# Kernel optimization log

Hardware: AMD Instinct MI355X
Metric: run time of the kernel (lower is better)

## Reference

```python
import jax, jax.numpy as jnp
import numpy as np

N = 50000
NEG_SLOPE = 0.2


def _gat_layer(x, src, dst, W, a_src, a_dst, b, heads, out_ch, concat):
    # x: [N, F_in]; W: [F_in, heads*out_ch]; a_src/a_dst: [heads, out_ch]; b: bias
    h = (x @ W).reshape(N, heads, out_ch)                      # [N,H,C]
    s_src = jnp.einsum('nhc,hc->nh', h, a_src)                 # [N,H]
    s_dst = jnp.einsum('nhc,hc->nh', h, a_dst)                 # [N,H]
    e = jax.nn.leaky_relu(s_src[src] + s_dst[dst], NEG_SLOPE)  # [E,H]
    # segment softmax over edges sharing the same destination node
    m = jax.ops.segment_max(e, dst, num_segments=N)
    m = jax.lax.stop_gradient(jnp.where(jnp.isfinite(m), m, 0.0))
    w = jnp.exp(e - m[dst])
    denom = jax.ops.segment_sum(w, dst, num_segments=N)
    alpha = w / (denom[dst] + 1e-16)                           # [E,H]
    out = jax.ops.segment_sum(alpha[:, :, None] * h[src], dst, num_segments=N)  # [N,H,C]
    out = out.reshape(N, heads * out_ch) if concat else out.mean(axis=1)
    return out + b


def setup_inputs() -> dict:
    key = jax.random.key(0)
    ks = jax.random.split(key, 16)
    F_in, Hd, H1, H3, F_out = 128, 64, 4, 6, 64
    E = 800000
    x = jax.random.normal(ks[0], (N, F_in), dtype=jnp.float32)
    edge_index = jax.random.randint(ks[1], (2, E), 0, N, dtype=jnp.int64)

    def glorot(k, shape, fan_in):
        return jax.random.normal(k, shape, dtype=jnp.float32) * (1.0 / np.sqrt(fan_in))

    params = {
        'W1': glorot(ks[2], (F_in, H1 * Hd), F_in),
        'a1_src': glorot(ks[3], (H1, Hd), Hd),
        'a1_dst': glorot(ks[4], (H1, Hd), Hd),
        'b1': jnp.zeros((H1 * Hd,), dtype=jnp.float32),
        'W2': glorot(ks[5], (H1 * Hd, H1 * Hd), H1 * Hd),
        'a2_src': glorot(ks[6], (H1, Hd), Hd),
        'a2_dst': glorot(ks[7], (H1, Hd), Hd),
        'b2': jnp.zeros((H1 * Hd,), dtype=jnp.float32),
        'W3': glorot(ks[8], (H1 * Hd, H3 * F_out), H1 * Hd),
        'a3_src': glorot(ks[9], (H3, F_out), F_out),
        'a3_dst': glorot(ks[10], (H3, F_out), F_out),
        'b3': jnp.zeros((F_out,), dtype=jnp.float32),
    }
    return {'x': x, 'edge_index': edge_index, **params}


def reference(x, edge_index, W1, a1_src, a1_dst, b1, W2, a2_src, a2_dst, b2, W3, a3_src, a3_dst, b3):
    # PyG GATConv default add_self_loops=True
    loops = jnp.arange(N, dtype=edge_index.dtype)
    src = jnp.concatenate([edge_index[0], loops])
    dst = jnp.concatenate([edge_index[1], loops])
    x1 = jax.nn.elu(_gat_layer(x, src, dst, W1, a1_src, a1_dst, b1, heads=4, out_ch=64, concat=True))
    x2 = jax.nn.elu(_gat_layer(x1, src, dst, W2, a2_src, a2_dst, b2, heads=4, out_ch=64, concat=True))
    x3 = _gat_layer(x2, src, dst, W3, a3_src, a3_dst, b3, heads=6, out_ch=64, concat=False)
    return x3
```

## Files before the change

kernel.cpp:

```cpp
#include <hip/hip_runtime.h>
#include <hip/hip_bf16.h>
#include <hip/hip_fp16.h>
#include <math.h>

#define NNODES 50000

typedef __attribute__((ext_vector_type(8))) short short8v;
typedef __attribute__((ext_vector_type(4))) float f32x4;
typedef unsigned short ushort_t;
typedef unsigned int uint_t;

__device__ inline ushort_t f2bf_bits(float v) {
    union { __hip_bfloat16 b; ushort_t u; } c;
    c.b = __float2bfloat16(v);
    return c.u;
}
__device__ inline float bfbits2f(ushort_t u) {
    union { __hip_bfloat16 b; ushort_t u; } c;
    c.u = u;
    return __bfloat162float(c.b);
}
__device__ inline ushort_t f2h_bits(float v) {
    union { __half h; ushort_t u; } c;
    c.h = __float2half(v);
    return c.u;
}
__device__ inline void cvt2(uint_t u, float& a, float& b) {
    union { uint_t u; __half2 h; } c; c.u = u;
    a = __low2float(c.h); b = __high2float(c.h);
}
__device__ inline uint_t fmap(float f) {
    uint_t b = __float_as_uint(f);
    return (b & 0x80000000u) ? ~b : (b | 0x80000000u);
}
__device__ inline float funmap(uint_t u) {
    return __uint_as_float((u & 0x80000000u) ? (u & 0x7FFFFFFFu) : ~u);
}

__global__ __launch_bounds__(256)
void split_kernel(const float4* __restrict__ in, ushort4* __restrict__ hi,
                  ushort4* __restrict__ lo, int n4) {
    int i = blockIdx.x * blockDim.x + threadIdx.x;
    if (i >= n4) return;
    float4 v = in[i];
    ushort4 h, l;
    h.x = f2bf_bits(v.x); l.x = f2bf_bits(v.x - bfbits2f(h.x));
    h.y = f2bf_bits(v.y); l.y = f2bf_bits(v.y - bfbits2f(h.y));
    h.z = f2bf_bits(v.z); l.z = f2bf_bits(v.z - bfbits2f(h.z));
    h.w = f2bf_bits(v.w); l.w = f2bf_bits(v.w - bfbits2f(h.w));
    hi[i] = h; lo[i] = l;
}

__global__ __launch_bounds__(256)
void wprep_all(const float* __restrict__ W1, const float* __restrict__ W2,
               const float* __restrict__ W3,
               ushort_t* __restrict__ w1h, ushort_t* __restrict__ w1l,
               ushort_t* __restrict__ w2h, ushort_t* __restrict__ w2l,
               ushort_t* __restrict__ w3h, ushort_t* __restrict__ w3l) {
    int idx = blockIdx.x * blockDim.x + threadIdx.x;
    const float* W; ushort_t* hT; ushort_t* lT; int K, N;
    if (idx < 128 * 256) { W = W1; hT = w1h; lT = w1l; K = 128; N = 256; }
    else if (idx < 128 * 256 + 256 * 256) {
        idx -= 128 * 256; W = W2; hT = w2h; lT = w2l; K = 256; N = 256;
    } else {
        idx -= 128 * 256 + 256 * 256;
        if (idx >= 256 * 384) return;
        W = W3; hT = w3h; lT = w3l; K = 256; N = 384;
    }
    int k = idx / N, n = idx - k * N;
    float v = W[idx];
    ushort_t hb = f2bf_bits(v);
    hT[(size_t)n * K + k] = hb;
    lT[(size_t)n * K + k] = f2bf_bits(v - bfbits2f(hb));
}

template<int H>
__global__ __launch_bounds__(256)
void gemm_fused(const ushort_t* __restrict__ Ahi, const ushort_t* __restrict__ Alo,
                const ushort_t* __restrict__ Bhi, const ushort_t* __restrict__ Blo,
                ushort_t* __restrict__ h16, float* __restrict__ ssrc,
                float* __restrict__ sdst, uint_t* __restrict__ gmaxu,
                const float* __restrict__ a_src, const float* __restrict__ a_dst,
                int M, int K) {
    __shared__ char smem[32768];
    __shared__ float sSs[128][2], sDs[128][2];
    __shared__ uint_t gblk[2];

    const int tid = threadIdx.x;
    const int lane = tid & 63;
    const int wid = tid >> 6;
    const int wm = wid >> 1, wn = wid & 1;
    const int bm = blockIdx.y * 128;
    const int bn = blockIdx.x * 128;
    const int r15 = lane & 15;
    const int g4 = lane >> 4;

    if (tid < 128) { sSs[tid][0] = 0.f; sSs[tid][1] = 0.f;
                     sDs[tid][0] = 0.f; sDs[tid][1] = 0.f; }
    if (tid < 2) gblk[tid] = 0;

    char* As_hi = smem;
    char* As_lo = smem + 8192;
    char* Bs_hi = smem + 16384;
    char* Bs_lo = smem + 24576;

    const int srow = tid >> 1;
    const int sch  = (tid & 1) * 2;
    const size_t arow = (size_t)(bm + srow) * K;
    const size_t brow = (size_t)(bn + srow) * K;

    f32x4 acc[4][4] = {};

    for (int k0 = 0; k0 < K; k0 += 32) {
        short8v a0 = *(const short8v*)&Ahi[arow + k0 + sch * 8];
        short8v a1 = *(const short8v*)&Ahi[arow + k0 + sch * 8 + 8];
        short8v l0 = *(const short8v*)&Alo[arow + k0 + sch * 8];
        short8v l1 = *(const short8v*)&Alo[arow + k0 + sch * 8 + 8];
        short8v b0 = *(const short8v*)&Bhi[brow + k0 + sch * 8];
        short8v b1 = *(const short8v*)&Bhi[brow + k0 + sch * 8 + 8];
        short8v m0 = *(const short8v*)&Blo[brow + k0 + sch * 8];
        short8v m1 = *(const short8v*)&Blo[brow + k0 + sch * 8 + 8];
        __syncthreads();
        *(short8v*)(As_hi + sch * 2048 + srow * 16)       = a0;
        *(short8v*)(As_hi + (sch + 1) * 2048 + srow * 16) = a1;
        *(short8v*)(As_lo + sch * 2048 + srow * 16)       = l0;
        *(short8v*)(As_lo + (sch + 1) * 2048 + srow * 16) = l1;
        *(short8v*)(Bs_hi + sch * 2048 + srow * 16)       = b0;
        *(short8v*)(Bs_hi + (sch + 1) * 2048 + srow * 16) = b1;
        *(short8v*)(Bs_lo + sch * 2048 + srow * 16)       = m0;
        *(short8v*)(Bs_lo + (sch + 1) * 2048 + srow * 16) = m1;
        __syncthreads();

        short8v ah[4], al[4], bh[4], bl[4];
        #pragma unroll
        for (int mi = 0; mi < 4; ++mi) {
            int row = wm * 64 + mi * 16 + r15;
            ah[mi] = *(const short8v*)(As_hi + g4 * 2048 + row * 16);
            al[mi] = *(const short8v*)(As_lo + g4 * 2048 + row * 16);
        }
        #pragma unroll
        for (int nj = 0; nj < 4; ++nj) {
            int row = wn * 64 + nj * 16 + r15;
            bh[nj] = *(const short8v*)(Bs_hi + g4 * 2048 + row * 16);
            bl[nj] = *(const short8v*)(Bs_lo + g4 * 2048 + row * 16);
        }
        #pragma unroll
        for (int mi = 0; mi < 4; ++mi)
            #pragma unroll
            for (int nj = 0; nj < 4; ++nj) {
                acc[mi][nj] = __builtin_amdgcn_mfma_f32_16x16x32_bf16(ah[mi], bh[nj], acc[mi][nj], 0, 0, 0);
                acc[mi][nj] = __builtin_amdgcn_mfma_f32_16x16x32_bf16(ah[mi], bl[nj], acc[mi][nj], 0, 0, 0);
                acc[mi][nj] = __builtin_amdgcn_mfma_f32_16x16x32_bf16(al[mi], bh[nj], acc[mi][nj], 0, 0, 0);
            }
    }
    __syncthreads();

    ushort_t* h2 = (ushort_t*)smem;
    const int headg = (bn >> 6) + wn;
    float asv[4], adv[4];
    #pragma unroll
    for (int nj = 0; nj < 4; ++nj) {
        asv[nj] = a_src[headg * 64 + nj * 16 + r15];
        adv[nj] = a_dst[headg * 64 + nj * 16 + r15];
    }
    #pragma unroll
    for (int mi = 0; mi < 4; ++mi) {
        #pragma unroll
        for (int reg = 0; reg < 4; ++reg) {
            int row_l = wm * 64 + mi * 16 + g4 * 4 + reg;
            int csw = ((row_l >> 2) & 3) << 2;
            float pS = 0.f, pD = 0.f;
            #pragma unroll
            for (int nj = 0; nj < 4; ++nj) {
                float v = acc[mi][nj][reg];
                int col_l = wn * 64 + nj * 16 + r15;
                h2[row_l * 128 + (col_l ^ csw)] = f2h_bits(v);
                pS += v * asv[nj];
                pD += v * adv[nj];
            }
            #pragma unroll
            for (int off = 1; off < 16; off <<= 1) {
                pS += __shfl_xor(pS, off);
                pD += __shfl_xor(pD, off);
            }
            if (r15 == 0 && bm + row_l < M) {
                atomicAdd(&sSs[row_l][wn], pS);
                atomicAdd(&sDs[row_l][wn], pD);
            }
        }
    }
    __syncthreads();

    uint_t* plane = (uint_t*)h16 + (size_t)(bn >> 7) * ((size_t)NNODES * 64);
    for (int u = tid; u < 128 * 64; u += 256) {
        int n_l = u >> 6, c = u & 63;
        if (bm + n_l < M) {
            int csw = ((n_l >> 2) & 3) << 2;
            uint_t lo = h2[n_l * 128 + (c ^ csw)];
            uint_t hi = h2[n_l * 128 + 64 + (c ^ csw)];
            plane[(size_t)(bm + n_l) * 64 + c] = lo | (hi << 16);
        }
    }
    {
        int row = tid >> 1, hl = tid & 1;
        if (bm + row < M) {
            int hg = (bn >> 6) + hl;
            float vS = sSs[row][hl];
            ssrc[(size_t)(bm + row) * H + hg] = vS;
            sdst[(size_t)(bm + row) * H + hg] = sDs[row][hl];
            atomicMax(&gblk[hl], fmap(vS));
        }
    }
    __syncthreads();
    if (tid < 2) atomicMax(&gmaxu[(bn >> 6) + tid], gblk[tid]);
}

__global__ void deg_kernel(const int* __restrict__ ei, int E, int Nn,
                           int* __restrict__ deg) {
    int e = blockIdx.x * blockDim.x + threadIdx.x;
    int tot = E + Nn;
    if (e >= tot) return;
    int d = (e < E) ? ei[E + e] : (e - E);
    atomicAdd(&deg[d], 1);
}

__global__ __launch_bounds__(1024)
void scan1_kernel(const int* __restrict__ deg, int* __restrict__ offs,
                  int* __restrict__ bsum, int n) {
    __shared__ int sh[1024];
    int t = threadIdx.x;
    int i = blockIdx.x * 1024 + t;
    int v = (i < n) ? deg[i] : 0;
    sh[t] = v;
    __syncthreads();
    for (int off = 1; off < 1024; off <<= 1) {
        int add = (t >= off) ? sh[t - off] : 0;
        __syncthreads();
        sh[t] += add;
        __syncthreads();
    }
    if (i < n) offs[i + 1] = sh[t];
    if (t == 1023) bsum[blockIdx.x] = sh[1023];
}

__global__ __launch_bounds__(64)
void scan2_kernel(const int* __restrict__ bsum, int* __restrict__ bexcl, int nb) {
    int t = threadIdx.x;
    int v = (t < nb) ? bsum[t] : 0;
    int orig = v;
    #pragma unroll
    for (int off = 1; off < 64; off <<= 1) {
        int u = __shfl_up(v, off);
        if (t >= off) v += u;
    }
    if (t < nb) bexcl[t] = v - orig;
}

__global__ void scan3_kernel(const int* __restrict__ deg, int* __restrict__ offs,
                             const int* __restrict__ bexcl, int* __restrict__ cursor,
                             int n) {
    int i = blockIdx.x * blockDim.x + threadIdx.x;
    if (i == 0) offs[0] = 0;
    if (i < n) {
        int inc = offs[i + 1] + bexcl[i >> 10];
        offs[i + 1] = inc;
        cursor[i] = inc - deg[i];
    }
}

__global__ void scatter_kernel(const int* __restrict__ ei, int E, int Nn,
                               int* __restrict__ cursor, int* __restrict__ csr_src) {
    int e = blockIdx.x * blockDim.x + threadIdx.x;
    int tot = E + Nn;
    if (e >= tot) return;
    int s, d;
    if (e < E) { s = ei[e]; d = ei[E + e]; }
    else       { s = d = e - E; }
    int pos = atomicAdd(&cursor[d], 1);
    csr_src[pos] = s;
}

template<int H>
__device__ inline void loadS(const float* __restrict__ p, float* v) {
    if constexpr (H == 4) {
        float4 t = *(const float4*)p;
        v[0] = t.x; v[1] = t.y; v[2] = t.z; v[3] = t.w;
    } else {
        const float2* q = (const float2*)p;
        float2 a = q[0], b = q[1], c = q[2];
        v[0] = a.x; v[1] = a.y; v[2] = b.x; v[3] = b.y; v[4] = c.x; v[5] = c.y;
    }
}

template<int H>
__global__ __launch_bounds__(256)
void smw_kernel(const float* __restrict__ ssrc, const float* __restrict__ sdst,
                const uint_t* __restrict__ gmaxu, const int* __restrict__ offs,
                const int* __restrict__ csr, float* __restrict__ wbuf,
                float* __restrict__ rden, int Nn) {
    int wid = (blockIdx.x * blockDim.x + threadIdx.x) >> 6;
    int lane = threadIdx.x & 63;
    if (wid >= Nn) return;
    int beg = offs[wid], end = offs[wid + 1];
    float sd[H], mx[H], den[H];
    #pragma unroll
    for (int h = 0; h < H; ++h) {
        sd[h] = sdst[wid * H + h];
        float t = funmap(gmaxu[h]) + sd[h];
        mx[h] = t > 0.f ? t : 0.2f * t;
        den[h] = 0.f;
    }
    for (int i = beg + lane; i < end; i += 64) {
        int s = csr[i];
        float sv[H];
        loadS<H>(ssrc + (size_t)s * H, sv);
        #pragma unroll
        for (int h = 0; h < H; ++h) {
            float sc = sv[h] + sd[h];
            sc = sc > 0.f ? sc : 0.2f * sc;
            float w = __expf(sc - mx[h]);
            wbuf[(size_t)i * H + h] = w;
            den[h] += w;
        }
    }
    #pragma unroll
    for (int h = 0; h < H; ++h) {
        #pragma unroll
        for (int off = 32; off; off >>= 1) den[h] += __shfl_xor(den[h], off);
    }
    if (lane == 0) {
        #pragma unroll
        for (int h = 0; h < H; ++h) rden[wid * H + h] = 1.f / (den[h] + 1e-16f);
    }
}

template<int H, bool MEAN>
__global__ __launch_bounds__(256)
void agg_kernel(const ushort_t* __restrict__ h16, const float* __restrict__ wbuf,
                const float* __restrict__ rden, const int* __restrict__ offs,
                const int* __restrict__ csr, const float* __restrict__ bias,
                float* __restrict__ outf, ushort_t* __restrict__ ohi,
                ushort_t* __restrict__ olo, int Nn) {
    constexpr int P = H / 2;
    int wid = (blockIdx.x * blockDim.x + threadIdx.x) >> 6;
    int lane = threadIdx.x & 63;
    if (wid >= Nn) return;
    int beg = offs[wid], end = offs[wid + 1];
    const uint_t* up = (const uint_t*)h16;
    const size_t psz = (size_t)Nn * 64;

    constexpr int U = (H == 4) ? 8 : 4;
    float acc0[H] = {}, acc1[H] = {};
    int i = beg;
    for (; i + U <= end; i += U) {
        int s[U];
        #pragma unroll
        for (int j = 0; j < U; ++j) s[j] = csr[i + j];
        uint_t g[U][P];
        #pragma unroll
        for (int j = 0; j < U; ++j)
            #pragma unroll
            for (int p = 0; p < P; ++p)
                g[j][p] = up[(size_t)p * psz + (size_t)s[j] * 64 + lane];
        float w[U][H];
        #pragma unroll
        for (int j = 0; j < U; ++j) {
            if constexpr (H == 4) {
                float4 t = *(const float4*)&wbuf[(size_t)(i + j) * 4];
                w[j][0] = t.x; w[j][1] = t.y; w[j][2] = t.z; w[j][3] = t.w;
            } else {
                const float2* q = (const float2*)&wbuf[(size_t)(i + j) * 6];
                float2 a = q[0], b = q[1], c = q[2];
                w[j][0] = a.x; w[j][1] = a.y; w[j][2] = b.x;
                w[j][3] = b.y; w[j][4] = c.x; w[j][5] = c.y;
            }
        }
        #pragma unroll
        for (int j = 0; j < U; ++j) {
            float v[H];
            #pragma unroll
            for (int p = 0; p < P; ++p) cvt2(g[j][p], v[2 * p], v[2 * p + 1]);
            float* a = (j & 1) ? acc1 : acc0;
            #pragma unroll
            for (int h = 0; h < H; ++h) a[h] += w[j][h] * v[h];
        }
    }
    for (; i < end; ++i) {
        int s = csr[i];
        float v[H];
        #pragma unroll
        for (int p = 0; p < P; ++p) {
            uint_t g = up[(size_t)p * psz + (size_t)s * 64 + lane];
            cvt2(g, v[2 * p], v[2 * p + 1]);
        }
        #pragma unroll
        for (int h = 0; h < H; ++h) acc0[h] += wbuf[(size_t)i * H + h] * v[h];
    }

    if (!MEAN) {
        #pragma unroll
        for (int h = 0; h < H; ++h) {
            float val = (acc0[h] + acc1[h]) * rden[wid * H + h] + bias[h * 64 + lane];
            val = val > 0.f ? val : expm1f(val);
            size_t idx = (size_t)wid * (H * 64) + h * 64 + lane;
            ushort_t hb = f2bf_bits(val);
            ohi[idx] = hb;
            olo[idx] = f2bf_bits(val - bfbits2f(hb));
        }
    } else {
        float m = 0.f;
        #pragma unroll
        for (int h = 0; h < H; ++h) m += (acc0[h] + acc1[h]) * rden[wid * H + h];
        outf[(size_t)wid * 64 + lane] = m * (1.f / (float)H) + bias[lane];
    }
}

extern "C" void kernel_launch(void* const* d_in, const int* in_sizes, int n_in,
                              void* d_out, int out_size, void* d_ws, size_t ws_size,
                              hipStream_t stream) {
    const float* x     = (const float*)d_in[0];
    const int*   ei    = (const int*)d_in[1];
    const float* W1    = (const float*)d_in[2];
    const float* a1s   = (const float*)d_in[3];
    const float* a1d   = (const float*)d_in[4];
    const float* b1    = (const float*)d_in[5];
    const float* W2    = (const float*)d_in[6];
    const float* a2s   = (const float*)d_in[7];
    const float* a2d   = (const float*)d_in[8];
    const float* b2    = (const float*)d_in[9];
    const float* W3    = (const float*)d_in[10];
    const float* a3s   = (const float*)d_in[11];
    const float* a3d   = (const float*)d_in[12];
    const float* b3    = (const float*)d_in[13];
    float* out = (float*)d_out;

    const int Nn = NNODES;
    const int E  = in_sizes[1] / 2;
    const int Etot = E + Nn;

    char* p = (char*)d_ws;
    auto carve = [&](size_t bytes) {
        char* r = p;
        p += (bytes + 255) & ~(size_t)255;
        return (void*)r;
    };
    ushort_t* h16   = (ushort_t*)carve((size_t)Nn * 384 * 2);
    ushort_t* R1    = (ushort_t*)carve((size_t)Nn * 256 * 4);
    ushort_t* x_hi  = R1;
    ushort_t* x_lo  = R1 + (size_t)Nn * 128;
    ushort_t* x1_hi = R1;
    ushort_t* x1_lo = R1 + (size_t)Nn * 256;
    ushort_t* w1hi  = (ushort_t*)carve((size_t)128 * 256 * 2);
    ushort_t* w1lo  = (ushort_t*)carve((size_t)128 * 256 * 2);
    ushort_t* w2hi  = (ushort_t*)carve((size_t)256 * 256 * 2);
    ushort_t* w2lo  = (ushort_t*)carve((size_t)256 * 256 * 2);
    ushort_t* w3hi  = (ushort_t*)carve((size_t)256 * 384 * 2);
    ushort_t* w3lo  = (ushort_t*)carve((size_t)256 * 384 * 2);
    float* ssrc   = (float*)carve((size_t)Nn * 6 * 4);
    float* sdst   = (float*)carve((size_t)Nn * 6 * 4);
    float* rden   = (float*)carve((size_t)Nn * 6 * 4);
    float* wbuf   = (float*)carve((size_t)Etot * 6 * 4);
    int*   deg    = (int*)carve((size_t)Nn * 4);
    int*   offs   = (int*)carve((size_t)(Nn + 1) * 4);
    int*   cursor = (int*)carve((size_t)Nn * 4);
    int*   csr    = (int*)carve((size_t)Etot * 4);
    uint_t* gmaxu = (uint_t*)carve(18 * 4);
    int*   bsum   = (int*)carve(64 * 4);
    int*   bexcl  = (int*)carve(64 * 4);

    hipMemsetAsync(deg, 0, (size_t)Nn * 4, stream);
    hipMemsetAsync(gmaxu, 0, 18 * 4, stream);
    {
        int nb = (Etot + 255) / 256;
        int nsb = (Nn + 1023) / 1024;
        deg_kernel<<<nb, 256, 0, stream>>>(ei, E, Nn, deg);
        scan1_kernel<<<nsb, 1024, 0, stream>>>(deg, offs, bsum, Nn);
        scan2_kernel<<<1, 64, 0, stream>>>(bsum, bexcl, nsb);
        scan3_kernel<<<(Nn + 255) / 256, 256, 0, stream>>>(deg, offs, bexcl, cursor, Nn);
        scatter_kernel<<<nb, 256, 0, stream>>>(ei, E, Nn, cursor, csr);
    }

    {
        int n4 = Nn * 128 / 4;
        split_kernel<<<(n4 + 255) / 256, 256, 0, stream>>>(
            (const float4*)x, (ushort4*)x_hi, (ushort4*)x_lo, n4);
        int wtot = 128 * 256 + 256 * 256 + 256 * 384;
        wprep_all<<<(wtot + 255) / 256, 256, 0, stream>>>(W1, W2, W3, w1hi, w1lo,
                                                          w2hi, w2lo, w3hi, w3lo);
    }

    const int node_blocks = (Nn + 3) / 4;
    const int gemm_rows = (Nn + 127) / 128;

    {
        dim3 g(2, gemm_rows);
        gemm_fused<4><<<g, 256, 0, stream>>>(x_hi, x_lo, w1hi, w1lo, h16,
                                             ssrc, sdst, gmaxu + 0, a1s, a1d, Nn, 128);
        smw_kernel<4><<<node_blocks, 256, 0, stream>>>(ssrc, sdst, gmaxu + 0, offs, csr,
                                                       wbuf, rden, Nn);
        agg_kernel<4, false><<<node_blocks, 256, 0, stream>>>(h16, wbuf, rden, offs, csr, b1,
                                                              nullptr, x1_hi, x1_lo, Nn);
    }
    {
        dim3 g(2, gemm_rows);
        gemm_fused<4><<<g, 256, 0, stream>>>(x1_hi, x1_lo, w2hi, w2lo, h16,
                                             ssrc, sdst, gmaxu + 6, a2s, a2d, Nn, 256);
        smw_kernel<4><<<node_blocks, 256, 0, stream>>>(ssrc, sdst, gmaxu + 6, offs, csr,
                                                       wbuf, rden, Nn);
        agg_kernel<4, false><<<node_blocks, 256, 0, stream>>>(h16, wbuf, rden, offs, csr, b2,
                                                              nullptr, x1_hi, x1_lo, Nn);
    }
    {
        dim3 g(3, gemm_rows);
        gemm_fused<6><<<g, 256, 0, stream>>>(x1_hi, x1_lo, w3hi, w3lo, h16,
                                             ssrc, sdst, gmaxu + 12, a3s, a3d, Nn, 256);
        smw_kernel<6><<<node_blocks, 256, 0, stream>>>(ssrc, sdst, gmaxu + 12, offs, csr,
                                                       wbuf, rden, Nn);
        agg_kernel<6, true><<<node_blocks, 256, 0, stream>>>(h16, wbuf, rden, offs, csr, b3,
                                                             out, nullptr, nullptr, Nn);
    }
}
```

Measured before the change: 573.2 us.

## Fuse softmax weight computation into aggregation kernel, drop edge weight buffer

Removes the separate softmax-weight kernel and its per-edge weight buffer. The aggregation kernel now gathers the source score for each edge and computes the exponential weight and the denominator inline, then normalizes at the end. This removes a kernel launch per layer and the write and read-back of an E×H float buffer. In exchange, every lane of the wavefront recomputes the exp redundantly per edge and issues an extra gather of ssrc.

After: 621.5 us. 8.4% more time.

```diff
diff --git a/kernel.cpp b/kernel.cpp
--- a/kernel.cpp
+++ b/kernel.cpp
@@ -292,55 +292,13 @@
     }
 }
 
-template<int H>
-__global__ __launch_bounds__(256)
-void smw_kernel(const float* __restrict__ ssrc, const float* __restrict__ sdst,
-                const uint_t* __restrict__ gmaxu, const int* __restrict__ offs,
-                const int* __restrict__ csr, float* __restrict__ wbuf,
-                float* __restrict__ rden, int Nn) {
-    int wid = (blockIdx.x * blockDim.x + threadIdx.x) >> 6;
-    int lane = threadIdx.x & 63;
-    if (wid >= Nn) return;
-    int beg = offs[wid], end = offs[wid + 1];
-    float sd[H], mx[H], den[H];
-    #pragma unroll
-    for (int h = 0; h < H; ++h) {
-        sd[h] = sdst[wid * H + h];
-        float t = funmap(gmaxu[h]) + sd[h];
-        mx[h] = t > 0.f ? t : 0.2f * t;
-        den[h] = 0.f;
-    }
-    for (int i = beg + lane; i < end; i += 64) {
-        int s = csr[i];
-        float sv[H];
-        loadS<H>(ssrc + (size_t)s * H, sv);
-        #pragma unroll
-        for (int h = 0; h < H; ++h) {
-            float sc = sv[h] + sd[h];
-            sc = sc > 0.f ? sc : 0.2f * sc;
-            float w = __expf(sc - mx[h]);
-            wbuf[(size_t)i * H + h] = w;
-            den[h] += w;
-        }
-    }
-    #pragma unroll
-    for (int h = 0; h < H; ++h) {
-        #pragma unroll
-        for (int off = 32; off; off >>= 1) den[h] += __shfl_xor(den[h], off);
-    }
-    if (lane == 0) {
-        #pragma unroll
-        for (int h = 0; h < H; ++h) rden[wid * H + h] = 1.f / (den[h] + 1e-16f);
-    }
-}
-
 template<int H, bool MEAN>
 __global__ __launch_bounds__(256)
-void agg_kernel(const ushort_t* __restrict__ h16, const float* __restrict__ wbuf,
-                const float* __restrict__ rden, const int* __restrict__ offs,
-                const int* __restrict__ csr, const float* __restrict__ bias,
-                float* __restrict__ outf, ushort_t* __restrict__ ohi,
-                ushort_t* __restrict__ olo, int Nn) {
+void agg_kernel(const ushort_t* __restrict__ h16, const float* __restrict__ ssrc,
+                const float* __restrict__ sdst, const uint_t* __restrict__ gmaxu,
+                const int* __restrict__ offs, const int* __restrict__ csr,
+                const float* __restrict__ bias, float* __restrict__ outf,
+                ushort_t* __restrict__ ohi, ushort_t* __restrict__ olo, int Nn) {
     constexpr int P = H / 2;
     int wid = (blockIdx.x * blockDim.x + threadIdx.x) >> 6;
     int lane = threadIdx.x & 63;
@@ -349,8 +307,17 @@
     const uint_t* up = (const uint_t*)h16;
     const size_t psz = (size_t)Nn * 64;
 
+    float sd[H], mx[H];
+    #pragma unroll
+    for (int h = 0; h < H; ++h) {
+        sd[h] = sdst[wid * H + h];
+        float t = funmap(gmaxu[h]) + sd[h];
+        mx[h] = t > 0.f ? t : 0.2f * t;
+    }
+
     constexpr int U = (H == 4) ? 8 : 4;
     float acc0[H] = {}, acc1[H] = {};
+    float den0[H] = {}, den1[H] = {};
     int i = beg;
     for (; i + U <= end; i += U) {
         int s[U];
@@ -362,45 +329,50 @@
             #pragma unroll
             for (int p = 0; p < P; ++p)
                 g[j][p] = up[(size_t)p * psz + (size_t)s[j] * 64 + lane];
-        float w[U][H];
+        float sv[U][H];
+        #pragma unroll
+        for (int j = 0; j < U; ++j) loadS<H>(ssrc + (size_t)s[j] * H, sv[j]);
         #pragma unroll
         for (int j = 0; j < U; ++j) {
-            if constexpr (H == 4) {
-                float4 t = *(const float4*)&wbuf[(size_t)(i + j) * 4];
-                w[j][0] = t.x; w[j][1] = t.y; w[j][2] = t.z; w[j][3] = t.w;
-            } else {
-                const float2* q = (const float2*)&wbuf[(size_t)(i + j) * 6];
-                float2 a = q[0], b = q[1], c = q[2];
-                w[j][0] = a.x; w[j][1] = a.y; w[j][2] = b.x;
-                w[j][3] = b.y; w[j][4] = c.x; w[j][5] = c.y;
+            float w[H], v[H];
+            #pragma unroll
+            for (int h = 0; h < H; ++h) {
+                float sc = sv[j][h] + sd[h];
+                sc = sc > 0.f ? sc : 0.2f * sc;
+                w[h] = __expf(sc - mx[h]);
             }
-        }
-        #pragma unroll
-        for (int j = 0; j < U; ++j) {
-            float v[H];
             #pragma unroll
             for (int p = 0; p < P; ++p) cvt2(g[j][p], v[2 * p], v[2 * p + 1]);
             float* a = (j & 1) ? acc1 : acc0;
-            #pragma unroll
-            for (int h = 0; h < H; ++h) a[h] += w[j][h] * v[h];
+            float* d = (j & 1) ? den1 : den0;
+            #pragma unroll
+            for (int h = 0; h < H; ++h) { a[h] += w[h] * v[h]; d[h] += w[h]; }
         }
     }
     for (; i < end; ++i) {
         int s = csr[i];
-        float v[H];
+        float sv[H], v[H];
+        loadS<H>(ssrc + (size_t)s * H, sv);
         #pragma unroll
         for (int p = 0; p < P; ++p) {
             uint_t g = up[(size_t)p * psz + (size_t)s * 64 + lane];
             cvt2(g, v[2 * p], v[2 * p + 1]);
         }
         #pragma unroll
-        for (int h = 0; h < H; ++h) acc0[h] += wbuf[(size_t)i * H + h] * v[h];
+        for (int h = 0; h < H; ++h) {
+            float sc = sv[h] + sd[h];
+            sc = sc > 0.f ? sc : 0.2f * sc;
+            float w = __expf(sc - mx[h]);
+            acc0[h] += w * v[h];
+            den0[h] += w;
+        }
     }
 
     if (!MEAN) {
         #pragma unroll
         for (int h = 0; h < H; ++h) {
-            float val = (acc0[h] + acc1[h]) * rden[wid * H + h] + bias[h * 64 + lane];
+            float val = (acc0[h] + acc1[h]) / (den0[h] + den1[h] + 1e-16f)
+                        + bias[h * 64 + lane];
             val = val > 0.f ? val : expm1f(val);
             size_t idx = (size_t)wid * (H * 64) + h * 64 + lane;
             ushort_t hb = f2bf_bits(val);
@@ -410,7 +382,8 @@
     } else {
         float m = 0.f;
         #pragma unroll
-        for (int h = 0; h < H; ++h) m += (acc0[h] + acc1[h]) * rden[wid * H + h];
+        for (int h = 0; h < H; ++h)
+            m += (acc0[h] + acc1[h]) / (den0[h] + den1[h] + 1e-16f);
         outf[(size_t)wid * 64 + lane] = m * (1.f / (float)H) + bias[lane];
     }
 }
@@ -458,8 +431,6 @@
     ushort_t* w3lo  = (ushort_t*)carve((size_t)256 * 384 * 2);
     float* ssrc   = (float*)carve((size_t)Nn * 6 * 4);
     float* sdst   = (float*)carve((size_t)Nn * 6 * 4);
-    float* rden   = (float*)carve((size_t)Nn * 6 * 4);
-    float* wbuf   = (float*)carve((size_t)Etot * 6 * 4);
     int*   deg    = (int*)carve((size_t)Nn * 4);
     int*   offs   = (int*)carve((size_t)(Nn + 1) * 4);
     int*   cursor = (int*)carve((size_t)Nn * 4);
@@ -496,27 +467,24 @@
         dim3 g(2, gemm_rows);
         gemm_fused<4><<<g, 256, 0, stream>>>(x_hi, x_lo, w1hi, w1lo, h16,
                                              ssrc, sdst, gmaxu + 0, a1s, a1d, Nn, 128);
-        smw_kernel<4><<<node_blocks, 256, 0, stream>>>(ssrc, sdst, gmaxu + 0, offs, csr,
-                                                       wbuf, rden, Nn);
-        agg_kernel<4, false><<<node_blocks, 256, 0, stream>>>(h16, wbuf, rden, offs, csr, b1,
+        agg_kernel<4, false><<<node_blocks, 256, 0, stream>>>(h16, ssrc, sdst, gmaxu + 0,
+                                                              offs, csr, b1,
                                                               nullptr, x1_hi, x1_lo, Nn);
     }
     {
         dim3 g(2, gemm_rows);
         gemm_fused<4><<<g, 256, 0, stream>>>(x1_hi, x1_lo, w2hi, w2lo, h16,
                                              ssrc, sdst, gmaxu + 6, a2s, a2d, Nn, 256);
-        smw_kernel<4><<<node_blocks, 256, 0, stream>>>(ssrc, sdst, gmaxu + 6, offs, csr,
-                                                       wbuf, rden, Nn);
-        agg_kernel<4, false><<<node_blocks, 256, 0, stream>>>(h16, wbuf, rden, offs, csr, b2,
+        agg_kernel<4, false><<<node_blocks, 256, 0, stream>>>(h16, ssrc, sdst, gmaxu + 6,
+                                                              offs, csr, b2,
                                                               nullptr, x1_hi, x1_lo, Nn);
     }
     {
         dim3 g(3, gemm_rows);
         gemm_fused<6><<<g, 256, 0, stream>>>(x1_hi, x1_lo, w3hi, w3lo, h16,
                                              ssrc, sdst, gmaxu + 12, a3s, a3d, Nn, 256);
-        smw_kernel<6><<<node_blocks, 256, 0, stream>>>(ssrc, sdst, gmaxu + 12, offs, csr,
-                                                       wbuf, rden, Nn);
-        agg_kernel<6, true><<<node_blocks, 256, 0, stream>>>(h16, wbuf, rden, offs, csr, b3,
+        agg_kernel<6, true><<<node_blocks, 256, 0, stream>>>(h16, ssrc, sdst, gmaxu + 12,
+                                                             offs, csr, b3,
                                                              out, nullptr, nullptr, Nn);
     }
 }
```
